# Kernel optimization log

Measured on AMD Instinct MI355X. Metric: run time of the kernel, lower is better.

Reference implementation:

```python
import jax, jax.numpy as jnp
import numpy as np

E = 1024   # embed_dim
H = 16     # head_size
DH = E // H  # head_dim = 64
B, S = 2, 2048
SCALE = 1.0 / np.sqrt(E)  # original divides by sqrt(query.size(-1)) == sqrt(embed_dim)


def setup_inputs() -> dict:
    key = jax.random.key(0)
    ks = jax.random.split(key, 11)
    init = 0.02
    return {
        "query": jax.random.normal(ks[0], (B, S, E), dtype=jnp.float32),
        "key":   jax.random.normal(ks[1], (B, S, E), dtype=jnp.float32),
        "value": jax.random.normal(ks[2], (B, S, E), dtype=jnp.float32),
        # per-head projection weights, stacked over heads: [H, E, DH]
        "Wq": jax.random.normal(ks[3], (H, E, DH), dtype=jnp.float32) * init,
        "bq": jax.random.normal(ks[4], (H, DH), dtype=jnp.float32) * init,
        "Wk": jax.random.normal(ks[5], (H, E, DH), dtype=jnp.float32) * init,
        "bk": jax.random.normal(ks[6], (H, DH), dtype=jnp.float32) * init,
        "Wv": jax.random.normal(ks[7], (H, E, DH), dtype=jnp.float32) * init,
        "bv": jax.random.normal(ks[8], (H, DH), dtype=jnp.float32) * init,
        "Wo": jax.random.normal(ks[9], (E, E), dtype=jnp.float32) * init,
        "bo": jax.random.normal(ks[10], (E,), dtype=jnp.float32) * init,
    }


def reference(query, key, value, Wq, bq, Wk, bk, Wv, bv, Wo, bo):
    # per-head linear projections (vectorized over heads)
    q = jnp.einsum('bse,hed->bhsd', query, Wq) + bq[None, :, None, :]
    k = jnp.einsum('bse,hed->bhsd', key,   Wk) + bk[None, :, None, :]
    v = jnp.einsum('bse,hed->bhsd', value, Wv) + bv[None, :, None, :]
    # NOTE: original code scales by sqrt(embed_dim), not sqrt(head_dim)
    scores = jnp.einsum('bhqd,bhkd->bhqk', q, k) * SCALE
    weights = jax.nn.softmax(scores, axis=-1)
    out = jnp.einsum('bhqk,bhkd->bhqd', weights, v)  # [B,H,S,DH]
    # concat heads along last dim (head order == stacking order)
    out = out.transpose(0, 2, 1, 3).reshape(B, S, H * DH)
    return out @ Wo + bo
```

## Files before the change

### kernel.cpp

```cpp
#include <hip/hip_runtime.h>

typedef __bf16 bf16;
typedef __bf16 bf16x8 __attribute__((ext_vector_type(8)));
typedef __bf16 bf16x4 __attribute__((ext_vector_type(4)));
typedef __bf16 bf16x2 __attribute__((ext_vector_type(2)));
typedef float f32x4 __attribute__((ext_vector_type(4)));

#define MM 4096
#define NN 1024
#define KK 1024

__device__ __forceinline__ void gload_lds16(const void* g, void* l) {
  __builtin_amdgcn_global_load_lds(
      (const __attribute__((address_space(1))) void*)g,
      (__attribute__((address_space(3))) void*)l, 16, 0, 0);
}

__global__ __launch_bounds__(256) void cvt_all(const float* __restrict__ q,
                                               const float* __restrict__ k,
                                               const float* __restrict__ v,
                                               const float* __restrict__ Wq,
                                               const float* __restrict__ Wk,
                                               const float* __restrict__ Wv,
                                               const float* __restrict__ Wo,
                                               bf16* __restrict__ Xb,
                                               bf16* __restrict__ Wt,
                                               bf16* __restrict__ Wot)
{
  __shared__ bf16 Sl[64 * 72];
  const int bid = blockIdx.x;
  const int t = threadIdx.x;

  if (bid < 12288) {
    int p = bid >> 12, bx = bid & 4095;
    const float* src = (p == 0) ? q : (p == 1 ? k : v);
    bf16* dst = Xb + (size_t)p * (MM * (size_t)KK);
    int i = (bx * 256 + t) * 4;
    float4 val = *(const float4*)(src + i);
    bf16x4 o;
    o.x = (bf16)val.x; o.y = (bf16)val.y; o.z = (bf16)val.z; o.w = (bf16)val.w;
    *(bf16x4*)(dst + i) = o;
    return;
  }

  const int wb = bid - 12288;
  const int p = wb >> 8, t8 = wb & 255;
  const int ti = t >> 4, c4 = (t & 15) * 4;

  if (p < 3) {
    const float* W = (p == 0) ? Wq : (p == 1 ? Wk : Wv);
    const int h = t8 >> 4, e0 = (t8 & 15) << 6;
#pragma unroll
    for (int r = 0; r < 4; ++r) {
      int e_l = r * 16 + ti;
      float4 val = *(const float4*)(W + (h << 16) + (e0 + e_l) * 64 + c4);
      bf16x4 o; o.x = (bf16)val.x; o.y = (bf16)val.y; o.z = (bf16)val.z; o.w = (bf16)val.w;
      *(bf16x4*)(Sl + e_l * 72 + c4) = o;
    }
    __syncthreads();
#pragma unroll
    for (int r = 0; r < 4; ++r) {
      int d_l = r * 16 + ti;
      bf16x4 o;
      o.x = Sl[(c4 + 0) * 72 + d_l];
      o.y = Sl[(c4 + 1) * 72 + d_l];
      o.z = Sl[(c4 + 2) * 72 + d_l];
      o.w = Sl[(c4 + 3) * 72 + d_l];
      *(bf16x4*)(Wt + (size_t)p * 1048576 + (size_t)((h << 6) + d_l) * 1024 + e0 + c4) = o;
    }
  } else {
    const int n0 = (t8 >> 4) << 6, k0 = (t8 & 15) << 6;
#pragma unroll
    for (int r = 0; r < 4; ++r) {
      int k_l = r * 16 + ti;
      float4 val = *(const float4*)(Wo + (size_t)(k0 + k_l) * 1024 + n0 + c4);
      bf16x4 o; o.x = (bf16)val.x; o.y = (bf16)val.y; o.z = (bf16)val.z; o.w = (bf16)val.w;
      *(bf16x4*)(Sl + k_l * 72 + c4) = o;
    }
    __syncthreads();
#pragma unroll
    for (int r = 0; r < 4; ++r) {
      int n_l = r * 16 + ti;
      bf16x4 o;
      o.x = Sl[(c4 + 0) * 72 + n_l];
      o.y = Sl[(c4 + 1) * 72 + n_l];
      o.z = Sl[(c4 + 2) * 72 + n_l];
      o.w = Sl[(c4 + 3) * 72 + n_l];
      *(bf16x4*)(Wot + (size_t)(n0 + n_l) * 1024 + k0 + c4) = o;
    }
  }
}

__device__ __forceinline__ void gemm_body(const bf16* __restrict__ A,
                                          const bf16* __restrict__ Bt,
                                          bf16* As, bf16* Bs,
                                          int m0, int n0, f32x4 (&acc)[4][4])
{
  const int tid = threadIdx.x;
  const int w = tid >> 6, L = tid & 63;
  const int quad = L >> 4, l16 = L & 15;
  const int wm = (w & 1) << 6, wn = (w >> 1) << 6;

  const bf16* Ag = A + (size_t)(m0 + w * 32 + (L >> 2)) * KK + (L & 3) * 8;
  const bf16* Bg = Bt + (size_t)(n0 + w * 32 + (L >> 2)) * KK + (L & 3) * 8;
  bf16* Al = As + w * 1024;
  bf16* Bl = Bs + w * 1024;

  for (int kt = 0; kt < KK / 32; ++kt) {
    __syncthreads();
    const bf16* a0 = Ag + kt * 32;
    const bf16* b0 = Bg + kt * 32;
    gload_lds16(a0, Al);
    gload_lds16(a0 + 16 * KK, Al + 512);
    gload_lds16(b0, Bl);
    gload_lds16(b0 + 16 * KK, Bl + 512);
    __syncthreads();
    bf16x8 af[4], bfr[4];
#pragma unroll
    for (int mi = 0; mi < 4; ++mi)
      af[mi] = *(const bf16x8*)(As + (wm + mi * 16 + l16) * 32 + quad * 8);
#pragma unroll
    for (int ni = 0; ni < 4; ++ni)
      bfr[ni] = *(const bf16x8*)(Bs + (wn + ni * 16 + l16) * 32 + quad * 8);
#pragma unroll
    for (int mi = 0; mi < 4; ++mi)
#pragma unroll
      for (int ni = 0; ni < 4; ++ni)
        acc[mi][ni] = __builtin_amdgcn_mfma_f32_16x16x32_bf16(af[mi], bfr[ni],
                                                              acc[mi][ni], 0, 0, 0);
  }
}

__global__ __launch_bounds__(256) void gemm_proj(const bf16* __restrict__ X,
                                                 const bf16* __restrict__ Wt,
                                                 const float* __restrict__ b0,
                                                 const float* __restrict__ b1,
                                                 const float* __restrict__ b2,
                                                 bf16* __restrict__ Out)
{
  __shared__ bf16 As[4096], Bs[4096];
  int p = blockIdx.y;
  const bf16* A = X + (size_t)p * 4194304;
  const bf16* Bt = Wt + (size_t)p * 1048576;
  const float* bias = (p == 0) ? b0 : (p == 1 ? b1 : b2);
  bf16* C = Out + (size_t)p * 4194304;
  int bx = blockIdx.x;
  int m0 = (bx >> 3) << 7, n0 = (bx & 7) << 7;
  f32x4 acc[4][4] = {};
  gemm_body(A, Bt, As, Bs, m0, n0, acc);
  const int L = threadIdx.x & 63, w = threadIdx.x >> 6;
  const int quad = L >> 4, l16 = L & 15;
  const int wm = (w & 1) << 6, wn = (w >> 1) << 6;
#pragma unroll
  for (int ni = 0; ni < 4; ++ni) {
    int col = n0 + wn + ni * 16 + l16;
    float bv = bias[col];
#pragma unroll
    for (int mi = 0; mi < 4; ++mi)
#pragma unroll
      for (int r = 0; r < 4; ++r) {
        int row = m0 + wm + mi * 16 + quad * 4 + r;
        C[(size_t)row * NN + col] = (bf16)(acc[mi][ni][r] + bv);
      }
  }
}

__global__ __launch_bounds__(256) void gemm_outp(const bf16* __restrict__ A,
                                                 const bf16* __restrict__ Bt,
                                                 const float* __restrict__ bias,
                                                 float* __restrict__ C)
{
  __shared__ bf16 As[2048], Bs[4096];
  const int bx = blockIdx.x;
  const int m0 = (bx >> 3) << 6, n0 = (bx & 7) << 7;
  const int tid = threadIdx.x;
  const int w = tid >> 6, L = tid & 63;
  const int quad = L >> 4, l16 = L & 15;
  const int wm = (w & 1) << 5, wn = (w >> 1) << 6;

  const bf16* Ag = A + (size_t)(m0 + w * 16 + (L >> 2)) * KK + (L & 3) * 8;
  const bf16* Bg = Bt + (size_t)(n0 + w * 32 + (L >> 2)) * KK + (L & 3) * 8;
  bf16* Al = As + w * 512;
  bf16* Bl = Bs + w * 1024;

  f32x4 acc[2][4] = {};
  for (int kt = 0; kt < KK / 32; ++kt) {
    __syncthreads();
    const bf16* a0 = Ag + kt * 32;
    const bf16* b0 = Bg + kt * 32;
    gload_lds16(a0, Al);
    gload_lds16(b0, Bl);
    gload_lds16(b0 + 16 * KK, Bl + 512);
    __syncthreads();
    bf16x8 af[2], bfr[4];
#pragma unroll
    for (int mi = 0; mi < 2; ++mi)
      af[mi] = *(const bf16x8*)(As + (wm + mi * 16 + l16) * 32 + quad * 8);
#pragma unroll
    for (int ni = 0; ni < 4; ++ni)
      bfr[ni] = *(const bf16x8*)(Bs + (wn + ni * 16 + l16) * 32 + quad * 8);
#pragma unroll
    for (int mi = 0; mi < 2; ++mi)
#pragma unroll
      for (int ni = 0; ni < 4; ++ni)
        acc[mi][ni] = __builtin_amdgcn_mfma_f32_16x16x32_bf16(af[mi], bfr[ni],
                                                              acc[mi][ni], 0, 0, 0);
  }

#pragma unroll
  for (int ni = 0; ni < 4; ++ni) {
    int col = n0 + wn + ni * 16 + l16;
    float bv = bias[col];
#pragma unroll
    for (int mi = 0; mi < 2; ++mi)
#pragma unroll
      for (int r = 0; r < 4; ++r) {
        int row = m0 + wm + mi * 16 + quad * 4 + r;
        C[(size_t)row * NN + col] = acc[mi][ni][r] + bv;
      }
  }
}

__global__ __launch_bounds__(256) void flash_attn(const bf16* __restrict__ Qm,
                                                  const bf16* __restrict__ Km,
                                                  const bf16* __restrict__ Vm,
                                                  bf16* __restrict__ Om)
{
  __shared__ bf16 Kl[64 * 72];
  __shared__ bf16 Vt[64 * 72];
  __shared__ bf16 Pl[4][16 * 72];
  const int tid = threadIdx.x;
  const int w = tid >> 6, L = tid & 63;
  const int quad = L >> 4, l16 = L & 15;
  const int qb = blockIdx.x & 31;
  const int bh = blockIdx.x >> 5;
  const int b = bh >> 4, h = bh & 15;
  const int s0 = qb << 6;
  const size_t base = (size_t)b * 2048 * 1024 + h * 64;

  const bf16* qp = Qm + base + (size_t)(s0 + w * 16 + l16) * 1024 + quad * 8;
  bf16x8 qf0 = *(const bf16x8*)qp;
  bf16x8 qf1 = *(const bf16x8*)(qp + 32);
  const float SL = 0.03125f * 1.44269504088896f;
#pragma unroll
  for (int j = 0; j < 8; ++j) {
    qf0[j] = (bf16)((float)qf0[j] * SL);
    qf1[j] = (bf16)((float)qf1[j] * SL);
  }

  float l_i[4] = {0.f, 0.f, 0.f, 0.f};
  f32x4 oacc[4] = {};

  const bf16* Kg = Km + base + (size_t)L * 1024 + w * 16;
  const int p = L & 31;
  const int kp = (p & 15) | ((p >> 4) << 5);
  const int dh8 = w * 16 + ((L >> 5) << 3);
  const int skp = ((kp & 15) << 2) | (kp >> 4);
  const bf16* Vg0 = Vm + base + (size_t)kp * 1024 + dh8;
  const bf16* Vg1 = Vg0 + 16 * 1024;

  bf16x8 k0 = *(const bf16x8*)Kg;
  bf16x8 k1 = *(const bf16x8*)(Kg + 8);
  bf16x8 va = *(const bf16x8*)Vg0;
  bf16x8 vb = *(const bf16x8*)Vg1;

  for (int kt = 0; kt < 32; ++kt) {
    __syncthreads();
    *(bf16x8*)(Kl + L * 72 + w * 16) = k0;
    *(bf16x8*)(Kl + L * 72 + w * 16 + 8) = k1;
#pragma unroll
    for (int j = 0; j < 8; ++j) {
      bf16x2 pr; pr.x = va[j]; pr.y = vb[j];
      *(bf16x2*)(Vt + (dh8 + j) * 72 + skp) = pr;
    }
    if (kt + 1 < 32) {
      k0 = *(const bf16x8*)(Kg + (size_t)(kt + 1) * 65536);
      k1 = *(const bf16x8*)(Kg + (size_t)(kt + 1) * 65536 + 8);
      va = *(const bf16x8*)(Vg0 + (size_t)(kt + 1) * 65536);
      vb = *(const bf16x8*)(Vg1 + (size_t)(kt + 1) * 65536);
    }
    __syncthreads();

    f32x4 sacc[4];
#pragma unroll
    for (int ns = 0; ns < 4; ++ns) {
      bf16x8 kf0 = *(const bf16x8*)(Kl + (ns * 16 + l16) * 72 + quad * 8);
      bf16x8 kf1 = *(const bf16x8*)(Kl + (ns * 16 + l16) * 72 + 32 + quad * 8);
      f32x4 s = {0.f, 0.f, 0.f, 0.f};
      s = __builtin_amdgcn_mfma_f32_16x16x32_bf16(qf0, kf0, s, 0, 0, 0);
      s = __builtin_amdgcn_mfma_f32_16x16x32_bf16(qf1, kf1, s, 0, 0, 0);
      sacc[ns] = s;
    }

#pragma unroll
    for (int r = 0; r < 4; ++r) {
      float p0 = __builtin_amdgcn_exp2f(sacc[0][r]);
      float p1 = __builtin_amdgcn_exp2f(sacc[1][r]);
      float p2 = __builtin_amdgcn_exp2f(sacc[2][r]);
      float p3 = __builtin_amdgcn_exp2f(sacc[3][r]);
      l_i[r] += (p0 + p1) + (p2 + p3);
      bf16x4 pv;
      pv.x = (bf16)p0; pv.y = (bf16)p1; pv.z = (bf16)p2; pv.w = (bf16)p3;
      *(bf16x4*)(&Pl[w][(quad * 4 + r) * 72 + l16 * 4]) = pv;
    }
    asm volatile("s_waitcnt lgkmcnt(0)" ::: "memory");
    bf16x8 pf0 = *(const bf16x8*)(&Pl[w][l16 * 72 + quad * 8]);
    bf16x8 pf1 = *(const bf16x8*)(&Pl[w][l16 * 72 + 32 + quad * 8]);
#pragma unroll
    for (int ds = 0; ds < 4; ++ds) {
      bf16x8 vf0 = *(const bf16x8*)(Vt + (ds * 16 + l16) * 72 + quad * 8);
      bf16x8 vf1 = *(const bf16x8*)(Vt + (ds * 16 + l16) * 72 + 32 + quad * 8);
      oacc[ds] = __builtin_amdgcn_mfma_f32_16x16x32_bf16(pf0, vf0, oacc[ds], 0, 0, 0);
      oacc[ds] = __builtin_amdgcn_mfma_f32_16x16x32_bf16(pf1, vf1, oacc[ds], 0, 0, 0);
    }
  }

#pragma unroll
  for (int r = 0; r < 4; ++r) {
    float l = l_i[r];
    l += __shfl_xor(l, 1);
    l += __shfl_xor(l, 2);
    l += __shfl_xor(l, 4);
    l += __shfl_xor(l, 8);
    float inv = 1.f / l;
    bf16* op = Om + base + (size_t)(s0 + w * 16 + quad * 4 + r) * 1024;
#pragma unroll
    for (int ds = 0; ds < 4; ++ds)
      op[ds * 16 + l16] = (bf16)(oacc[ds][r] * inv);
  }
}

extern "C" void kernel_launch(void* const* d_in, const int* in_sizes, int n_in,
                              void* d_out, int out_size, void* d_ws, size_t ws_size,
                              hipStream_t stream)
{
  const float* q  = (const float*)d_in[0];
  const float* k  = (const float*)d_in[1];
  const float* v  = (const float*)d_in[2];
  const float* Wq = (const float*)d_in[3];
  const float* bq = (const float*)d_in[4];
  const float* Wk = (const float*)d_in[5];
  const float* bk = (const float*)d_in[6];
  const float* Wv = (const float*)d_in[7];
  const float* bv = (const float*)d_in[8];
  const float* Wo = (const float*)d_in[9];
  const float* bo = (const float*)d_in[10];

  char* ws = (char*)d_ws;
  bf16* Xb  = (bf16*)ws;
  bf16* Wt  = (bf16*)(ws + 25165824);
  bf16* Wot = (bf16*)(ws + 31457280);
  bf16* QKV = (bf16*)(ws + 33554432);
  bf16* O   = (bf16*)ws;

  cvt_all<<<dim3(13312), 256, 0, stream>>>(q, k, v, Wq, Wk, Wv, Wo, Xb, Wt, Wot);
  gemm_proj<<<dim3(256, 3), 256, 0, stream>>>(Xb, Wt, bq, bk, bv, QKV);
  flash_attn<<<dim3(1024), 256, 0, stream>>>(QKV, QKV + 4194304, QKV + 8388608, O);
  gemm_outp<<<dim3(512), 256, 0, stream>>>(O, Wot, bo, (float*)d_out);
}
```

Baseline: 247.6 us.

## Rework flash attention around 32x32 MFMA with 128-row query tiles and swizzled LDS

The attention kernel now uses 32x32x16 MFMA instructions, with each wave handling 32 query rows, so a block covers 128 queries and the grid is halved. This doubles reuse of each K/V tile loaded into LDS. Padded LDS rows are replaced by an XOR swizzle to avoid bank conflicts. The row sum is computed by an extra MFMA against a ones vector instead of VALU adds and shuffles. The cost is fewer blocks (512) for occupancy, more accumulator registers, and extra MFMA work for the sums.

```diff
diff --git a/kernel.cpp b/kernel.cpp
--- a/kernel.cpp
+++ b/kernel.cpp
@@ -5,6 +5,7 @@
 typedef __bf16 bf16x4 __attribute__((ext_vector_type(4)));
 typedef __bf16 bf16x2 __attribute__((ext_vector_type(2)));
 typedef float f32x4 __attribute__((ext_vector_type(4)));
+typedef float f32x16 __attribute__((ext_vector_type(16)));
 
 #define MM 4096
 #define NN 1024
@@ -226,107 +227,104 @@
                                                   const bf16* __restrict__ Vm,
                                                   bf16* __restrict__ Om)
 {
-  __shared__ bf16 Kl[64 * 72];
-  __shared__ bf16 Vt[64 * 72];
-  __shared__ bf16 Pl[4][16 * 72];
+  __shared__ bf16 Kl[64 * 64];
+  __shared__ bf16 Vt[64 * 64];
+  __shared__ bf16 Pl[4][32 * 64];
+
   const int tid = threadIdx.x;
   const int w = tid >> 6, L = tid & 63;
-  const int quad = L >> 4, l16 = L & 15;
-  const int qb = blockIdx.x & 31;
-  const int bh = blockIdx.x >> 5;
+  const int l32 = L & 31, hi = L >> 5;
+  const int bh = blockIdx.x & 31;
+  const int qb = blockIdx.x >> 5;
   const int b = bh >> 4, h = bh & 15;
-  const int s0 = qb << 6;
-  const size_t base = (size_t)b * 2048 * 1024 + h * 64;
-
-  const bf16* qp = Qm + base + (size_t)(s0 + w * 16 + l16) * 1024 + quad * 8;
-  bf16x8 qf0 = *(const bf16x8*)qp;
-  bf16x8 qf1 = *(const bf16x8*)(qp + 32);
+  const int s0 = qb << 7;
+  const size_t base = (size_t)b * 2097152 + h * 64;
+
+  bf16x8 qf[4];
   const float SL = 0.03125f * 1.44269504088896f;
-#pragma unroll
-  for (int j = 0; j < 8; ++j) {
-    qf0[j] = (bf16)((float)qf0[j] * SL);
-    qf1[j] = (bf16)((float)qf1[j] * SL);
-  }
-
-  float l_i[4] = {0.f, 0.f, 0.f, 0.f};
-  f32x4 oacc[4] = {};
-
-  const bf16* Kg = Km + base + (size_t)L * 1024 + w * 16;
-  const int p = L & 31;
-  const int kp = (p & 15) | ((p >> 4) << 5);
-  const int dh8 = w * 16 + ((L >> 5) << 3);
-  const int skp = ((kp & 15) << 2) | (kp >> 4);
-  const bf16* Vg0 = Vm + base + (size_t)kp * 1024 + dh8;
-  const bf16* Vg1 = Vg0 + 16 * 1024;
+  {
+    const bf16* qp = Qm + base + (size_t)(s0 + w * 32 + l32) * 1024 + hi * 8;
+#pragma unroll
+    for (int s = 0; s < 4; ++s) {
+      bf16x8 tq = *(const bf16x8*)(qp + s * 16);
+#pragma unroll
+      for (int j = 0; j < 8; ++j) tq[j] = (bf16)((float)tq[j] * SL);
+      qf[s] = tq;
+    }
+  }
+
+  bf16x8 onesf;
+#pragma unroll
+  for (int j = 0; j < 8; ++j) onesf[j] = (bf16)1.0f;
+
+  f32x16 oacc0 = {}, oacc1 = {}, lacc = {};
+
+  const bf16* Kg = Km + base + (size_t)(2 * l32 + hi) * 1024 + w * 16;
+  const int dh8 = w * 16 + hi * 8;
+  const bf16* Vg = Vm + base + (size_t)(2 * l32) * 1024 + dh8;
+  bf16* Pw = &Pl[w][0];
+  const int r7 = l32 & 7;
 
   bf16x8 k0 = *(const bf16x8*)Kg;
   bf16x8 k1 = *(const bf16x8*)(Kg + 8);
-  bf16x8 va = *(const bf16x8*)Vg0;
-  bf16x8 vb = *(const bf16x8*)Vg1;
+  bf16x8 va = *(const bf16x8*)Vg;
+  bf16x8 vb = *(const bf16x8*)(Vg + 1024);
 
   for (int kt = 0; kt < 32; ++kt) {
     __syncthreads();
-    *(bf16x8*)(Kl + L * 72 + w * 16) = k0;
-    *(bf16x8*)(Kl + L * 72 + w * 16 + 8) = k1;
+    *(bf16x8*)(Kl + L * 64 + ((((2 * w + 0) ^ (L & 7)) << 3))) = k0;
+    *(bf16x8*)(Kl + L * 64 + ((((2 * w + 1) ^ (L & 7)) << 3))) = k1;
 #pragma unroll
     for (int j = 0; j < 8; ++j) {
+      int row = dh8 + j;
       bf16x2 pr; pr.x = va[j]; pr.y = vb[j];
-      *(bf16x2*)(Vt + (dh8 + j) * 72 + skp) = pr;
+      *(bf16x2*)(Vt + row * 64 + (((l32 >> 2) ^ (row & 7)) << 3) + ((l32 & 3) << 1)) = pr;
     }
     if (kt + 1 < 32) {
       k0 = *(const bf16x8*)(Kg + (size_t)(kt + 1) * 65536);
       k1 = *(const bf16x8*)(Kg + (size_t)(kt + 1) * 65536 + 8);
-      va = *(const bf16x8*)(Vg0 + (size_t)(kt + 1) * 65536);
-      vb = *(const bf16x8*)(Vg1 + (size_t)(kt + 1) * 65536);
-    }
-    __syncthreads();
-
-    f32x4 sacc[4];
-#pragma unroll
-    for (int ns = 0; ns < 4; ++ns) {
-      bf16x8 kf0 = *(const bf16x8*)(Kl + (ns * 16 + l16) * 72 + quad * 8);
-      bf16x8 kf1 = *(const bf16x8*)(Kl + (ns * 16 + l16) * 72 + 32 + quad * 8);
-      f32x4 s = {0.f, 0.f, 0.f, 0.f};
-      s = __builtin_amdgcn_mfma_f32_16x16x32_bf16(qf0, kf0, s, 0, 0, 0);
-      s = __builtin_amdgcn_mfma_f32_16x16x32_bf16(qf1, kf1, s, 0, 0, 0);
-      sacc[ns] = s;
-    }
-
-#pragma unroll
-    for (int r = 0; r < 4; ++r) {
-      float p0 = __builtin_amdgcn_exp2f(sacc[0][r]);
-      float p1 = __builtin_amdgcn_exp2f(sacc[1][r]);
-      float p2 = __builtin_amdgcn_exp2f(sacc[2][r]);
-      float p3 = __builtin_amdgcn_exp2f(sacc[3][r]);
-      l_i[r] += (p0 + p1) + (p2 + p3);
-      bf16x4 pv;
-      pv.x = (bf16)p0; pv.y = (bf16)p1; pv.z = (bf16)p2; pv.w = (bf16)p3;
-      *(bf16x4*)(&Pl[w][(quad * 4 + r) * 72 + l16 * 4]) = pv;
+      va = *(const bf16x8*)(Vg + (size_t)(kt + 1) * 65536);
+      vb = *(const bf16x8*)(Vg + (size_t)(kt + 1) * 65536 + 1024);
+    }
+    __syncthreads();
+
+    f32x16 sa = {}, sb = {};
+#pragma unroll
+    for (int s = 0; s < 4; ++s) {
+      bf16x8 kfa = *(const bf16x8*)(Kl + (l32)      * 64 + (((2 * s + hi) ^ r7) << 3));
+      bf16x8 kfb = *(const bf16x8*)(Kl + (32 + l32) * 64 + (((2 * s + hi) ^ r7) << 3));
+      sa = __builtin_amdgcn_mfma_f32_32x32x16_bf16(qf[s], kfa, sa, 0, 0, 0);
+      sb = __builtin_amdgcn_mfma_f32_32x32x16_bf16(qf[s], kfb, sb, 0, 0, 0);
+    }
+
+#pragma unroll
+    for (int reg = 0; reg < 16; ++reg) {
+      int row = (reg & 3) + ((reg >> 2) << 3) + (hi << 2);
+      float p0 = __builtin_amdgcn_exp2f(sa[reg]);
+      float p1 = __builtin_amdgcn_exp2f(sb[reg]);
+      bf16x2 pv; pv.x = (bf16)p0; pv.y = (bf16)p1;
+      *(bf16x2*)(Pw + row * 64 + (((l32 >> 2) ^ (row & 7)) << 3) + ((l32 & 3) << 1)) = pv;
     }
     asm volatile("s_waitcnt lgkmcnt(0)" ::: "memory");
-    bf16x8 pf0 = *(const bf16x8*)(&Pl[w][l16 * 72 + quad * 8]);
-    bf16x8 pf1 = *(const bf16x8*)(&Pl[w][l16 * 72 + 32 + quad * 8]);
-#pragma unroll
-    for (int ds = 0; ds < 4; ++ds) {
-      bf16x8 vf0 = *(const bf16x8*)(Vt + (ds * 16 + l16) * 72 + quad * 8);
-      bf16x8 vf1 = *(const bf16x8*)(Vt + (ds * 16 + l16) * 72 + 32 + quad * 8);
-      oacc[ds] = __builtin_amdgcn_mfma_f32_16x16x32_bf16(pf0, vf0, oacc[ds], 0, 0, 0);
-      oacc[ds] = __builtin_amdgcn_mfma_f32_16x16x32_bf16(pf1, vf1, oacc[ds], 0, 0, 0);
-    }
-  }
-
-#pragma unroll
-  for (int r = 0; r < 4; ++r) {
-    float l = l_i[r];
-    l += __shfl_xor(l, 1);
-    l += __shfl_xor(l, 2);
-    l += __shfl_xor(l, 4);
-    l += __shfl_xor(l, 8);
-    float inv = 1.f / l;
-    bf16* op = Om + base + (size_t)(s0 + w * 16 + quad * 4 + r) * 1024;
-#pragma unroll
-    for (int ds = 0; ds < 4; ++ds)
-      op[ds * 16 + l16] = (bf16)(oacc[ds][r] * inv);
+
+#pragma unroll
+    for (int s = 0; s < 4; ++s) {
+      bf16x8 paf = *(const bf16x8*)(Pw + l32 * 64 + (((2 * s + hi) ^ r7) << 3));
+      bf16x8 vf0 = *(const bf16x8*)(Vt + (l32)      * 64 + (((2 * s + hi) ^ r7) << 3));
+      bf16x8 vf1 = *(const bf16x8*)(Vt + (32 + l32) * 64 + (((2 * s + hi) ^ r7) << 3));
+      oacc0 = __builtin_amdgcn_mfma_f32_32x32x16_bf16(paf, vf0, oacc0, 0, 0, 0);
+      oacc1 = __builtin_amdgcn_mfma_f32_32x32x16_bf16(paf, vf1, oacc1, 0, 0, 0);
+      lacc  = __builtin_amdgcn_mfma_f32_32x32x16_bf16(paf, onesf, lacc, 0, 0, 0);
+    }
+  }
+
+#pragma unroll
+  for (int reg = 0; reg < 16; ++reg) {
+    int row = (reg & 3) + ((reg >> 2) << 3) + (hi << 2);
+    float inv = 1.f / lacc[reg];
+    bf16* op = Om + base + (size_t)(s0 + w * 32 + row) * 1024;
+    op[l32]      = (bf16)(oacc0[reg] * inv);
+    op[32 + l32] = (bf16)(oacc1[reg] * inv);
   }
 }
 
@@ -355,6 +353,6 @@
 
   cvt_all<<<dim3(13312), 256, 0, stream>>>(q, k, v, Wq, Wk, Wv, Wo, Xb, Wt, Wot);
   gemm_proj<<<dim3(256, 3), 256, 0, stream>>>(Xb, Wt, bq, bk, bv, QKV);
-  flash_attn<<<dim3(1024), 256, 0, stream>>>(QKV, QKV + 4194304, QKV + 8388608, O);
+  flash_attn<<<dim3(512), 256, 0, stream>>>(QKV, QKV + 4194304, QKV + 8388608, O);
   gemm_outp<<<dim3(512), 256, 0, stream>>>(O, Wot, bo, (float*)d_out);
 }
```

New measurement: 229.7 us. -7.2%, faster.
